# Performance work log

Measured on AMD Instinct MI355X. Metric: run time of the kernel, lower is better.

Reference implementation:

```python
import jax, jax.numpy as jnp
import numpy as np

B, T = 16, 100
MCL = 100      # MAX_CODE_LEN
D_IN = 200     # input_dim (= ques_encoding)
D_BERT = 768
KC = 50        # KC_one_hot_dim
KCD = 100      # kc_embed_dim
HID = 128
SCALE_BERT = 100
TW = 0.5       # QPALA_config.total_attention_weight
BTW = 0.5      # BLAA_config.total_attention_weight


def setup_inputs():
    key = jax.random.key(0)
    ks = jax.random.split(key, 20)
    f32 = jnp.float32
    # composite input feature vector: [ques_enc | code2vec idx | bert | time | score | kc one-hot]
    rnn_first = (jax.random.uniform(ks[0], (B, T, D_IN)) < 0.1).astype(f32)
    c2v = jax.random.randint(ks[1], (B, T, 3 * MCL), 0, 10000).astype(f32)
    bert = jax.random.normal(ks[2], (B, T, D_BERT), f32)
    time_f = jax.random.uniform(ks[3], (B, T, 10), f32)
    score_f = jax.random.uniform(ks[4], (B, T, 2), f32)
    kc = (jax.random.uniform(ks[5], (B, T, KC)) < 0.15).astype(f32)
    x = jnp.concatenate([rnn_first, c2v, bert, time_f, score_f, kc], axis=2)  # [B,T,1330]
    s = 0.05
    p = lambda k, shp: jax.random.normal(k, shp, f32) * s
    return dict(
        x=x,
        node_emb=p(ks[6], (10002, 100)),
        path_emb=p(ks[7], (20002, 100)),
        Wb=p(ks[8], (SCALE_BERT, D_BERT)), bb=jnp.zeros((SCALE_BERT,), f32),
        Wna=p(ks[9], (500, 500)), bna=jnp.zeros((500,), f32),
        Wia=p(ks[10], (KCD, 500)), bia=jnp.zeros((KCD,), f32),
        Wattn=p(ks[11], (1, 500)), battn=jnp.zeros((1,), f32),
        kc_emb=p(ks[12], (KC, KCD)),
        Wt=p(ks[13], (1, SCALE_BERT + KC + KCD)), bt=jnp.zeros((1,), f32),
        Wih=p(ks[14], (4 * HID, 950)), Whh=p(ks[15], (4 * HID, HID)),
        bih=jnp.zeros((4 * HID,), f32), bhh=jnp.zeros((4 * HID,), f32),
        Wfc=p(ks[16], (100, HID + KC + D_IN)), bfc=jnp.zeros((100,), f32),
    )


def _lstm(xseq, Wih, Whh, bih, bhh):
    # PyTorch LSTM, gate order i,f,g,o; batch_first
    bsz = xseq.shape[0]
    pre = jnp.einsum('btd,gd->btg', xseq, Wih) + bih + bhh  # [B,T,4H]

    def step(carry, g_in):
        h, c = carry
        g = g_in + h @ Whh.T
        i, f, gg, o = jnp.split(g, 4, axis=-1)
        c = jax.nn.sigmoid(f) * c + jax.nn.sigmoid(i) * jnp.tanh(gg)
        h = jax.nn.sigmoid(o) * jnp.tanh(c)
        return (h, c), h

    init = (jnp.zeros((bsz, HID), xseq.dtype), jnp.zeros((bsz, HID), xseq.dtype))
    _, hs = jax.lax.scan(step, init, jnp.swapaxes(pre, 0, 1))
    return jnp.swapaxes(hs, 0, 1)


def _forward(x, node_emb, path_emb, Wb, bb, Wna, bna, Wia, bia, Wattn, battn,
             kc_emb, Wt, bt, Wih, Whh, bih, bhh, Wfc, bfc):
    b, t = x.shape[0], x.shape[1]
    rnn_first = x[:, :, :D_IN]
    bert = x[:, :, 500:500 + D_BERT]
    kc_part = x[:, :, 1280:1280 + KC]
    c2v = x[:, :, D_IN:D_IN + 3 * MCL].reshape(b, t, MCL, 3).astype(jnp.int32)
    # gather embeddings + broadcast encoding -> full_embed [B,T,MCL,500]
    full = jnp.concatenate([
        node_emb[c2v[..., 0]], node_emb[c2v[..., 2]], path_emb[c2v[..., 1]],
        jnp.broadcast_to(rnn_first[:, :, None, :], (b, t, MCL, D_IN))], axis=3)
    bert_vec = bert @ Wb.T + bb  # [B,T,100]
    # non-interactive attention pooling (NB: original softmaxes over dim=1 = time)
    cw = jnp.tanh(full @ Wna.T + bna) @ Wattn.T + battn  # [B,T,MCL,1]
    aw = jax.nn.softmax(cw, axis=1)
    na = jnp.sum(full * aw, axis=2)  # [B,T,500]
    kcn = jnp.sum(kc_part, axis=2, keepdims=True)
    kcn = jnp.where(kcn == 0, 1.0, kcn)
    # interactive (KC) cross attention
    trans = full @ Wia.T + bia  # [B,T,MCL,KCD]
    Q = kc_part[..., None] * kc_emb[None, None]  # [B,T,KC,KCD]
    attn = jax.nn.softmax(jnp.einsum('btkd,btmd->btkm', Q, trans), axis=-1)
    Hm = jnp.einsum('btkm,btmd->btkd', attn, trans) * kc_part[..., None]
    ia = jnp.sum(Hm, axis=2) / kcn  # [B,T,KCD]
    rnn_input = jnp.concatenate([kc_part, rnn_first, ia, na, bert_vec], axis=2)  # [B,T,950]
    lstm_out = _lstm(rnn_input, Wih, Whh, bih, bhh)  # [B,T,HID]
    # per-time-step causal attention over lstm_out (vectorized form of the python loop)
    w = (jnp.concatenate([bert_vec, kc_part, ia], axis=2) @ Wt.T + bt)[..., 0]  # [B,T]
    mask = jnp.tril(jnp.ones((t, t), bool))
    logits = jnp.where(mask[None], w[:, None, :], -1e30)
    cattn = jax.nn.softmax(logits, axis=-1)  # [B,T,T]
    cur = jnp.einsum('bij,bjh->bih', cattn, lstm_out)
    attended = lstm_out * (1.0 - TW)
    attended = attended.at[:, 0].set(lstm_out[:, 0])
    idx = jnp.arange(t)
    addm = ((idx >= 1) & (idx <= t - 2)).astype(x.dtype)[None, :, None]
    attended = attended + cur * BTW * addm
    out = jax.nn.sigmoid(
        jnp.concatenate([rnn_first, kc_part, attended], axis=2) @ Wfc.T + bfc)
    return out  # [B,T,100]


def reference(x, node_emb, path_emb, Wb, bb, Wna, bna, Wia, bia, Wattn, battn,
              kc_emb, Wt, bt, Wih, Whh, bih, bhh, Wfc, bfc):
    return _forward(x, node_emb, path_emb, Wb, bb, Wna, bna, Wia, bia, Wattn, battn,
                    kc_emb, Wt, bt, Wih, Whh, bih, bhh, Wfc, bfc)
```

## Files before the change

### kernel.cpp

```cpp
#include <hip/hip_runtime.h>
#include <math.h>

typedef unsigned short ushort_t;
typedef unsigned char uchar_t;
typedef __attribute__((ext_vector_type(8))) short bf16x8;
typedef __attribute__((ext_vector_type(4))) float f32x4;

constexpr int CB = 16, CT = 100, CMCL = 100, CDIN = 200;
constexpr int CKC = 50, CHID = 128;
constexpr int XCH = 1330;
constexpr int NBT = CB * CT;
constexpr int NNODE = 10002, NPATH = 20002;
constexpr int TRS = 114;
constexpr int HSTR = 136;
constexpr int NT8_W = 1024;
constexpr int NTF_W = 384;
constexpr int PT8_W = 512;
constexpr int PTF_W = 256;
constexpr int XR_W  = 640;

__device__ __forceinline__ float frcp(float v){ return __builtin_amdgcn_rcpf(v); }
__device__ __forceinline__ float fsigmoid(float v){ return frcp(1.f + __expf(-v)); }
__device__ __forceinline__ float ftanh_(float v){
  float e = __expf(-2.f*fabsf(v));
  return copysignf((1.f - e) * frcp(1.f + e), v);
}
__device__ __forceinline__ float wredsum(float v){
  #pragma unroll
  for (int off = 32; off; off >>= 1) v += __shfl_xor(v, off);
  return v;
}
__device__ __forceinline__ float wredmax(float v){
  #pragma unroll
  for (int off = 32; off; off >>= 1) v = fmaxf(v, __shfl_xor(v, off));
  return v;
}
__device__ __forceinline__ ushort_t f2b(float f){
  union { float f; unsigned u; } c{f};
  return (ushort_t)((c.u + 0x7FFFu + ((c.u >> 16) & 1u)) >> 16);
}
__device__ __forceinline__ float b2f(unsigned hbits){
  union { unsigned u; float f; } c{hbits << 16};
  return c.f;
}
__device__ __forceinline__ void b8f(const ushort_t* p, float* o){
  uint4 v = *reinterpret_cast<const uint4*>(p);
  o[0]=b2f(v.x & 0xFFFFu); o[1]=b2f(v.x >> 16);
  o[2]=b2f(v.y & 0xFFFFu); o[3]=b2f(v.y >> 16);
  o[4]=b2f(v.z & 0xFFFFu); o[5]=b2f(v.z >> 16);
  o[6]=b2f(v.w & 0xFFFFu); o[7]=b2f(v.w >> 16);
}
__device__ __forceinline__ uchar_t ff8(float f){
  union { float f; unsigned u; } c{f};
  unsigned s = (c.u >> 24) & 0x80u;
  unsigned a = c.u & 0x7FFFFFFFu;
  a = a < 0x3C000000u ? 0x3C000000u : a;
  a = a + 0x0007FFFFu + ((a >> 20) & 1u);
  a = a > 0x43E00000u ? 0x43E00000u : a;
  return (uchar_t)(s | (((a >> 20) - 0x3C0u) & 0x7Fu));
}
__device__ __forceinline__ void f8x8f(uint2 p, float* o){
  #pragma unroll
  for (int h = 0; h < 2; ++h) {
    unsigned w = h ? p.y : p.x;
    unsigned d0 = (w & 0xFFu) | ((w & 0xFF00u) << 8);
    unsigned d1 = ((w >> 16) & 0xFFu) | ((w >> 8) & 0x00FF0000u);
    unsigned v0 = ((d0 & 0x00800080u) << 8) | (((d0 & 0x007F007Fu) << 4) + 0x3C003C00u);
    unsigned v1 = ((d1 & 0x00800080u) << 8) | (((d1 & 0x007F007Fu) << 4) + 0x3C003C00u);
    union { unsigned u; float f; } c0{v0 << 16}, c1{v0 & 0xFFFF0000u}, c2{v1 << 16}, c3{v1 & 0xFFFF0000u};
    o[4*h+0] = c0.f; o[4*h+1] = c1.f; o[4*h+2] = c2.f; o[4*h+3] = c3.f;
  }
}

struct GDesc {
  const float* A; const float* B; float* Cf; void* Cb;
  int lda, kOff, kMax, K, M, Npad, rbp, cb, nsplit, ldc, omode, blocks;
};
struct MegaArgs { GDesc d[6]; int nd; };

__global__ __launch_bounds__(256) void mega_gemm(MegaArgs args)
{
  constexpr int KS = 136;
  __shared__ ushort_t As[128*KS];
  __shared__ ushort_t Bs[128*KS];
  int id = blockIdx.x;
  int di = 0;
  while (di < args.nd-1 && id >= args.d[di].blocks) { id -= args.d[di].blocks; ++di; }
  GDesc g = args.d[di];
  const int per = g.rbp * g.cb;
  const int sp = id / per, r = id % per;
  const int xcd = r & 7, s2 = r >> 3;
  const int y = xcd + 8*(s2 / g.cb), cbi = s2 % g.cb;
  const int bm = y*128, bn = cbi*128;
  if (bm >= g.M) return;
  const int tid = threadIdx.x, lane = tid & 63, w = tid >> 6;
  const int wm = w & 1, wn = w >> 1;
  const int lr = lane & 15, lkq = lane >> 4;
  const int kbase = g.kOff + sp * g.K;
  const int hK = g.K >> 1;

  for (int f = tid; f < 128*hK; f += 256) {
    int row = f / hK, j2 = (f % hK)*2;
    int gm = bm + row;
    float2 va = make_float2(0.f,0.f);
    if (gm < g.M && kbase + j2 + 2 <= g.kMax)
      va = *reinterpret_cast<const float2*>(g.A + (long)gm*g.lda + kbase + j2);
    *reinterpret_cast<unsigned*>(&As[row*KS + j2]) = (unsigned)f2b(va.x) | ((unsigned)f2b(va.y)<<16);
    float2 vb = *reinterpret_cast<const float2*>(g.B + ((long)sp*g.Npad + bn + row)*g.K + j2);
    *reinterpret_cast<unsigned*>(&Bs[row*KS + j2]) = (unsigned)f2b(vb.x) | ((unsigned)f2b(vb.y)<<16);
  }
  const int padw = (128 - g.K) >> 1;
  for (int f = tid; f < 128*padw; f += 256) {
    int row = f / padw, jd = f % padw;
    *reinterpret_cast<unsigned*>(&As[row*KS + g.K + jd*2]) = 0u;
    *reinterpret_cast<unsigned*>(&Bs[row*KS + g.K + jd*2]) = 0u;
  }
  __syncthreads();

  f32x4 acc[4][4];
  #pragma unroll
  for (int i = 0; i < 4; ++i)
    #pragma unroll
    for (int j = 0; j < 4; ++j) acc[i][j] = f32x4{0.f,0.f,0.f,0.f};
  #pragma unroll
  for (int ks = 0; ks < 4; ++ks) {
    const int ko = ks*32 + lkq*8;
    bf16x8 af[4], bf[4];
    #pragma unroll
    for (int i = 0; i < 4; ++i)
      af[i] = *reinterpret_cast<const bf16x8*>(&As[(wm*64 + i*16 + lr)*KS + ko]);
    #pragma unroll
    for (int j = 0; j < 4; ++j)
      bf[j] = *reinterpret_cast<const bf16x8*>(&Bs[(wn*64 + j*16 + lr)*KS + ko]);
    #pragma unroll
    for (int i = 0; i < 4; ++i)
      #pragma unroll
      for (int j = 0; j < 4; ++j)
        acc[i][j] = __builtin_amdgcn_mfma_f32_16x16x32_bf16(af[i], bf[j], acc[i][j], 0, 0, 0);
  }
  #pragma unroll
  for (int i = 0; i < 4; ++i) {
    #pragma unroll
    for (int j = 0; j < 4; ++j) {
      #pragma unroll
      for (int rr = 0; rr < 4; ++rr) {
        int gr = bm + wm*64 + i*16 + lkq*4 + rr;
        int gc = bn + wn*64 + j*16 + lr;
        if (gr < g.M) {
          float v = acc[i][j][rr];
          if (g.omode == 2)      ((uchar_t*)g.Cb)[(long)gr * g.ldc + gc] = ff8(v);
          else if (g.omode == 1) ((ushort_t*)g.Cb)[(long)gr * g.ldc + gc] = f2b(v);
          else                   g.Cf[((long)sp*g.M + gr)*g.ldc + gc] = v;
        }
      }
    }
  }
}

constexpr long PK_E0 = 1024L*100;
constexpr long PK_E1 = PK_E0 + 384L*100;
constexpr long PK_E2 = PK_E1 + 512L*100;
constexpr long PK_E3 = PK_E2 + 256L*100;
constexpr long PK_E4 = PK_E3 + 2L*XR_W*100;
constexpr long PK_E5 = PK_E4 + 6L*128*128;
constexpr long PK_E6 = PK_E5 + 10L*512*96;
constexpr long PK_E7 = PK_E6 + 512;
constexpr long PK_E8 = PK_E7 + 378L*100;

__global__ void pack_all(
    const float* __restrict__ Wna, const float* __restrict__ Wia,
    const float* __restrict__ bna, const float* __restrict__ bia,
    const float* __restrict__ Wb, const float* __restrict__ Wih,
    const float* __restrict__ Wattn, const float* __restrict__ Wfc,
    float* __restrict__ Bn8, float* __restrict__ Bnb,
    float* __restrict__ Bp8, float* __restrict__ Bpb,
    float* __restrict__ XB2, float* __restrict__ bias_x,
    float* __restrict__ BertB, float* __restrict__ P2B,
    ushort_t* __restrict__ WAB, float* __restrict__ WfcT)
{
  long i = (long)blockIdx.x*256 + threadIdx.x;
  if (i < PK_E0) {
    int n = (int)(i / 100), k = (int)(i % 100);
    float v = 0.f;
    if (n < 500)                    v = Wna[(long)n*500 + k];
    else if (n >= 512 && n < 1012)  v = Wna[(long)(n-512)*500 + 100 + k];
    Bn8[i] = v;
  } else if (i < PK_E1) {
    long j = i - PK_E0;
    int n = (int)(j / 100), k = (int)(j % 100);
    float v = 0.f;
    if (n < 100)                    v = (k == n) ? 1.f : 0.f;
    else if (n >= 112 && n < 212)   v = Wia[(long)(n-112)*500 + k];
    else if (n >= 224 && n < 324)   v = Wia[(long)(n-224)*500 + 100 + k];
    Bnb[j] = v;
  } else if (i < PK_E2) {
    long j = i - PK_E1;
    int n = (int)(j / 100), k = (int)(j % 100);
    Bp8[j] = (n < 500) ? Wna[(long)n*500 + 200 + k] : 0.f;
  } else if (i < PK_E3) {
    long j = i - PK_E2;
    int n = (int)(j / 100), k = (int)(j % 100);
    float v = 0.f;
    if (n < 100)                    v = (k == n) ? 1.f : 0.f;
    else if (n >= 112 && n < 212)   v = Wia[(long)(n-112)*500 + 200 + k];
    Bpb[j] = v;
  } else if (i < PK_E4) {
    long j = i - PK_E3;
    if (j < XR_W) {
      float b = 0.f;
      if (j < 500) b = bna[j];
      else if (j >= 512 && j < 612) b = bia[j-512];
      bias_x[j] = b;
    }
    int s = (int)(j / (XR_W*100)), n = (int)((j / 100) % XR_W), k = (int)(j % 100);
    int k2 = s*100 + k;
    float v = 0.f;
    if (n < 500)                  v = Wna[(long)n*500 + 300 + k2];
    else if (n >= 512 && n < 612) v = Wia[(long)(n-512)*500 + 300 + k2];
    XB2[j] = v;
  } else if (i < PK_E5) {
    long j = i - PK_E4;
    int s = (int)(j / (128*128)), n = (int)((j / 128) % 128), k = (int)(j % 128);
    BertB[j] = (n < 100) ? Wb[(long)n*768 + s*128 + k] : 0.f;
  } else if (i < PK_E6) {
    long j = i - PK_E5;
    int s = (int)(j / (512*96)), n = (int)((j / 96) % 512), k = (int)(j % 96);
    int kg = s*96 + k;
    P2B[j] = (kg < 950) ? Wih[(long)n*950 + kg] : 0.f;
  } else if (i < PK_E7) {
    long j = i - PK_E6;
    WAB[j] = (j < 500) ? f2b(Wattn[j]) : (ushort_t)0;
  } else if (i < PK_E8) {
    long j = i - PK_E7;
    int o = (int)(j / 378), q = (int)(j % 378);
    WfcT[q*100 + o] = Wfc[j];
  }
}

__global__ __launch_bounds__(256) void reduce1(
    const float* __restrict__ xrP, const float* __restrict__ bias_x, ushort_t* __restrict__ XR,
    const float* __restrict__ bertP, const float* __restrict__ bb, float* __restrict__ rnn)
{
  int bt = blockIdx.x, tid = threadIdx.x;
  for (int c = tid; c < XR_W; c += 256) {
    float v = xrP[(long)bt*XR_W + c] + xrP[((long)NBT + bt)*XR_W + c] + bias_x[c];
    XR[(long)bt*XR_W + c] = f2b(v);
  }
  if (tid < 100) {
    float v = bb[tid];
    #pragma unroll
    for (int s = 0; s < 6; ++s) v += bertP[((long)s*NBT + bt)*128 + tid];
    rnn[(long)bt*950 + 850 + tid] = v;
  }
}

__global__ __launch_bounds__(512) void reduce_p2(
    const float* __restrict__ p2P, const float* __restrict__ bih, const float* __restrict__ bhh,
    ushort_t* __restrict__ P2)
{
  int bt = blockIdx.x, g = threadIdx.x;
  float v = bih[g] + bhh[g];
  #pragma unroll
  for (int s = 0; s < 10; ++s) v += p2P[((long)s*NBT + bt)*512 + g];
  int bq = bt / CT, tt = bt % CT;
  int q = g >> 7, rem = g & 127, ww = rem >> 4, lr2 = rem & 15;
  int lk2 = bq >> 2, rr = bq & 3;
  P2[((((long)tt*4 + q)*8 + ww)*4 + lk2)*64 + lr2*4 + rr] = f2b(v);
}

__global__ __launch_bounds__(256) void cw2_kernel(
    const float* __restrict__ x, const uchar_t* __restrict__ NT8,
    const uchar_t* __restrict__ PT8, const ushort_t* __restrict__ XR,
    const ushort_t* __restrict__ WAB,
    const float* __restrict__ battn, float* __restrict__ cwT)
{
  int bt = blockIdx.x, b = bt / CT, t = bt % CT;
  int tid = threadIdx.x, w = tid >> 6, lane = tid & 63;
  __shared__ int idx_s[300];
  for (int i = tid; i < 300; i += 256) idx_s[i] = (int)x[(long)bt*XCH + 200 + i];
  float rseg[8], wseg[8];
  b8f(XR + (long)bt*XR_W + lane*8, rseg);
  b8f(WAB + lane*8, wseg);
  __syncthreads();
  float bat = battn[0];

  uint2 A0, C0, P0, A1, C1, P1;
  auto issue = [&](int m, uint2& A, uint2& C, uint2& P){
    if (m < CMCL) {
      int ai = idx_s[3*m], pi = idx_s[3*m+1], ci = idx_s[3*m+2];
      A = *reinterpret_cast<const uint2*>(NT8 + (long)ai*NT8_W + lane*8);
      C = *reinterpret_cast<const uint2*>(NT8 + (long)ci*NT8_W + 512 + lane*8);
      P = *reinterpret_cast<const uint2*>(PT8 + (long)pi*PT8_W + lane*8);
    }
  };
  auto proc = [&](int m, const uint2& A, const uint2& C, const uint2& P){
    if (m >= CMCL) return;
    float fa[8], fc[8], fp[8];
    f8x8f(A, fa); f8x8f(C, fc); f8x8f(P, fp);
    float acc = 0.f;
    #pragma unroll
    for (int j = 0; j < 8; ++j)
      acc = fmaf(ftanh_(fa[j] + fc[j] + fp[j] + rseg[j]), wseg[j], acc);
    acc = wredsum(acc);
    if (lane == 0) cwT[((long)b*CMCL + m)*CT + t] = acc + bat;
  };

  issue(w, A0, C0, P0);
  for (int it = 0; it < 25; it += 2) {
    int m0 = w + it*4;
    issue(m0 + 4, A1, C1, P1);
    proc(m0, A0, C0, P0);
    issue(m0 + 8, A0, C0, P0);
    proc(m0 + 4, A1, C1, P1);
  }
}

__global__ void aw_kernel(const float* __restrict__ cwT, float* __restrict__ awT)
{
  int bm = blockIdx.x; int lane = threadIdx.x;
  const float* row = cwT + (long)bm * CT;
  bool h1 = lane < (CT - 64);
  float v0 = row[lane];
  float v1 = h1 ? row[64 + lane] : -3.0e38f;
  float mx = wredmax(fmaxf(v0, v1));
  float e0 = __expf(v0 - mx);
  float e1 = h1 ? __expf(v1 - mx) : 0.f;
  float s = wredsum(e0 + e1);
  float inv = frcp(s);
  awT[(long)bm*CT + lane] = e0 * inv;
  if (h1) awT[(long)bm*CT + 64 + lane] = e1 * inv;
}

__global__ __launch_bounds__(256) void fuse2_kernel(
    const float* __restrict__ x,
    const uchar_t* __restrict__ NTF, const uchar_t* __restrict__ PTF,
    const ushort_t* __restrict__ XR, const float* __restrict__ awT,
    const float* __restrict__ kc_emb, float* __restrict__ rnn,
    const float* __restrict__ Wt, const float* __restrict__ bt0, float* __restrict__ wbuf)
{
  int bt = blockIdx.x, b = bt / CT, t = bt % CT;
  int tid = threadIdx.x, w = tid >> 6, lane = tid & 63;
  int sub = lane >> 5, li = lane & 31;

  __shared__ ushort_t tr_s[100*TRS];
  __shared__ float nacc[4][344];
  __shared__ float ia_red[4][104];
  __shared__ float ia_f[100];
  __shared__ float aw_s[100];
  __shared__ int   idx_s[300];
  __shared__ float kcl[CKC];
  __shared__ int   act_k[CKC];
  __shared__ int   nact_s;
  __shared__ float kcn_s, awsum_s;

  for (int i = tid; i < 300; i += 256) idx_s[i] = (int)x[(long)bt*XCH + 200 + i];
  if (tid < 100) aw_s[tid] = awT[((long)b*CMCL + tid)*CT + t];
  if (tid < CKC) kcl[tid] = x[(long)bt*XCH + 1280 + tid];
  __syncthreads();
  if (tid == 0) {
    float kcn = 0.f; int na = 0;
    for (int k = 0; k < CKC; ++k) { float v = kcl[k]; kcn += v; if (v != 0.f) act_k[na++] = k; }
    nact_s = na; kcn_s = (kcn == 0.f) ? 1.f : kcn;
    float s = 0.f;
    for (int m = 0; m < CMCL; ++m) s += aw_s[m];
    awsum_s = s;
  }
  float rwseg[8];
  if (li >= 14 && li < 28) b8f(XR + (long)bt*XR_W + 512 + (li-14)*8, rwseg);
  __syncthreads();

  float na_a[8] = {}, na_c[8] = {}, na_p[8] = {};
  const bool gv = (li < 28);
  uint2 A0, C0, P0, A1, C1, P1;
  auto g_issue = [&](int m, uint2& A, uint2& C, uint2& P){
    if (m < CMCL && gv) {
      int ai = idx_s[3*m], pi = idx_s[3*m+1], ci = idx_s[3*m+2];
      int offA = li*8;
      int offC = li*8 + ((li < 14) ? 0 : 112);
      A = *reinterpret_cast<const uint2*>(NTF + (long)ai*NTF_W + offA);
      C = *reinterpret_cast<const uint2*>(NTF + (long)ci*NTF_W + offC);
      P = *reinterpret_cast<const uint2*>(PTF + (long)pi*PTF_W + offA);
    }
  };
  auto g_proc = [&](int m, const uint2& A, const uint2& C, const uint2& P){
    if (m >= CMCL || !gv) return;
    float fa[8], fc[8], fp[8];
    f8x8f(A, fa); f8x8f(C, fc); f8x8f(P, fp);
    if (li < 14) {
      float awm = aw_s[m];
      #pragma unroll
      for (int j = 0; j < 8; ++j) {
        na_a[j] = fmaf(awm, fa[j], na_a[j]);
        na_c[j] = fmaf(awm, fc[j], na_c[j]);
        na_p[j] = fmaf(awm, fp[j], na_p[j]);
      }
    } else {
      unsigned* d32 = reinterpret_cast<unsigned*>(&tr_s[m*TRS + (li-14)*8]);
      #pragma unroll
      for (int jj = 0; jj < 4; ++jj) {
        float lo = fa[2*jj]   + fc[2*jj]   + fp[2*jj]   + rwseg[2*jj];
        float hi = fa[2*jj+1] + fc[2*jj+1] + fp[2*jj+1] + rwseg[2*jj+1];
        d32[jj] = (unsigned)f2b(lo) | ((unsigned)f2b(hi) << 16);
      }
    }
  };
  const int mb = w*2 + sub;
  g_issue(mb, A0, C0, P0);
  for (int it = 0; it < 13; it += 2) {
    g_issue((it+1)*8 + mb, A1, C1, P1);
    g_proc(it*8 + mb, A0, C0, P0);
    g_issue((it+2)*8 + mb, A0, C0, P0);
    g_proc((it+1)*8 + mb, A1, C1, P1);
  }
  #pragma unroll
  for (int j = 0; j < 8; ++j) {
    na_a[j] += __shfl_xor(na_a[j], 32);
    na_c[j] += __shfl_xor(na_c[j], 32);
    na_p[j] += __shfl_xor(na_p[j], 32);
  }
  if (lane < 14) {
    #pragma unroll
    for (int j = 0; j < 8; ++j) {
      nacc[w][      lane*8 + j] = na_a[j];
      nacc[w][112 + lane*8 + j] = na_c[j];
      nacc[w][224 + lane*8 + j] = na_p[j];
    }
  }
  __syncthreads();

  for (int q = tid; q < 336; q += 256) {
    float v = nacc[0][q] + nacc[1][q] + nacc[2][q] + nacc[3][q];
    int seg = q / 112, col = q % 112;
    if (col < 100) rnn[(long)bt*950 + 350 + seg*100 + col] = v;
  }
  for (int q = tid; q < CDIN; q += 256) {
    float xv = x[(long)bt*XCH + q];
    rnn[(long)bt*950 + 50 + q] = xv;
    rnn[(long)bt*950 + 650 + q] = awsum_s * xv;
  }
  if (tid < CKC) rnn[(long)bt*950 + tid] = kcl[tid];

  float ia0 = 0.f, ia1 = 0.f;
  const bool vrow1 = lane < 36;
  const bool vpv   = lane < 50;
  const int nact = nact_s;
  const unsigned* tr32_0 = reinterpret_cast<const unsigned*>(&tr_s[lane*TRS]);
  const unsigned* tr32_1 = reinterpret_cast<const unsigned*>(&tr_s[(64+lane)*TRS]);
  const unsigned* tr32   = reinterpret_cast<const unsigned*>(tr_s);
  for (int ki = w; ki < nact; ki += 4) {
    int k = act_k[ki];
    float kck = kcl[k];
    const float* ke = kc_emb + (long)k*100;
    float s0 = 0.f, s1 = 0.f;
    #pragma unroll 5
    for (int dh = 0; dh < 50; ++dh) {
      float k0 = ke[2*dh], k1 = ke[2*dh+1];
      unsigned u0 = tr32_0[dh];
      s0 = fmaf(k0, b2f(u0 & 0xffffu), s0);
      s0 = fmaf(k1, b2f(u0 >> 16), s0);
      if (vrow1) {
        unsigned u1 = tr32_1[dh];
        s1 = fmaf(k0, b2f(u1 & 0xffffu), s1);
        s1 = fmaf(k1, b2f(u1 >> 16), s1);
      }
    }
    s0 *= kck; s1 *= kck;
    float mx = wredmax(fmaxf(s0, vrow1 ? s1 : -3.0e38f));
    float p0e = __expf(s0 - mx);
    float p1e = vrow1 ? __expf(s1 - mx) : 0.f;
    float sm = wredsum(p0e + p1e);
    float inv = kck * frcp(sm);
    p0e *= inv; p1e *= inv;
    #pragma unroll 4
    for (int m = 0; m < CMCL; ++m) {
      float pm = (m < 64) ? __shfl(p0e, m) : __shfl(p1e, m - 64);
      if (vpv) {
        unsigned u = tr32[m*57 + lane];
        ia0 = fmaf(pm, b2f(u & 0xffffu), ia0);
        ia1 = fmaf(pm, b2f(u >> 16), ia1);
      }
    }
  }
  if (vpv) { ia_red[w][2*lane] = ia0; ia_red[w][2*lane+1] = ia1; }
  __syncthreads();
  if (tid < 100) {
    float v = (ia_red[0][tid] + ia_red[1][tid] + ia_red[2][tid] + ia_red[3][tid]) * frcp(kcn_s);
    rnn[(long)bt*950 + 250 + tid] = v;
    ia_f[tid] = v;
  }
  __syncthreads();
  if (tid < 64) {
    float acc = 0.f;
    for (int i = tid; i < 250; i += 64) {
      float f;
      if (i < 100)      f = rnn[(long)bt*950 + 850 + i];
      else if (i < 150) f = kcl[i - 100];
      else              f = ia_f[i - 150];
      acc = fmaf(Wt[i], f, acc);
    }
    acc = wredsum(acc);
    if (tid == 0) wbuf[bt] = acc + bt0[0];
  }
}

__global__ __launch_bounds__(512) void lstm_mfma2(
    const ushort_t* __restrict__ P2,
    const float* __restrict__ Whh,
    float* __restrict__ lstm_out)
{
  const int tid = threadIdx.x, lane = tid & 63, w = tid >> 6;
  const int lr = lane & 15, lkq = lane >> 4;
  __shared__ ushort_t H[2][16 * HSTR];
  {
    ushort_t* hp = &H[0][0];
    for (int i = tid; i < 2*16*HSTR; i += 512) hp[i] = 0;
  }

  bf16x8 bw0[4], bw1[4], bw2[4], bw3[4];
  #pragma unroll
  for (int kk = 0; kk < 4; ++kk) {
    short s[8];
    const float* wp0 = Whh + (long)(0*128 + w*16 + lr) * 128 + kk*32 + lkq*8;
    const float* wp1 = Whh + (long)(1*128 + w*16 + lr) * 128 + kk*32 + lkq*8;
    const float* wp2 = Whh + (long)(2*128 + w*16 + lr) * 128 + kk*32 + lkq*8;
    const float* wp3 = Whh + (long)(3*128 + w*16 + lr) * 128 + kk*32 + lkq*8;
    #pragma unroll
    for (int j = 0; j < 8; ++j) s[j] = (short)f2b(wp0[j]);
    bw0[kk] = bf16x8{s[0],s[1],s[2],s[3],s[4],s[5],s[6],s[7]};
    #pragma unroll
    for (int j = 0; j < 8; ++j) s[j] = (short)f2b(wp1[j]);
    bw1[kk] = bf16x8{s[0],s[1],s[2],s[3],s[4],s[5],s[6],s[7]};
    #pragma unroll
    for (int j = 0; j < 8; ++j) s[j] = (short)f2b(wp2[j]);
    bw2[kk] = bf16x8{s[0],s[1],s[2],s[3],s[4],s[5],s[6],s[7]};
    #pragma unroll
    for (int j = 0; j < 8; ++j) s[j] = (short)f2b(wp3[j]);
    bw3[kk] = bf16x8{s[0],s[1],s[2],s[3],s[4],s[5],s[6],s[7]};
  }

  auto pptr = [&](int t, int q){
    return reinterpret_cast<const uint2*>(P2 + (((((long)t*4 + q)*8 + w)*4 + lkq)*64 + lr*4));
  };
  uint2 pc0 = *pptr(0,0), pc1 = *pptr(0,1), pc2 = *pptr(0,2), pc3 = *pptr(0,3);
  uint2 pn0, pn1, pn2, pn3;
  f32x4 c = {0.f,0.f,0.f,0.f};
  __syncthreads();

  int pb = 0;
  for (int t = 0; t < CT; ++t) {
    if (t + 1 < CT) { pn0 = *pptr(t+1,0); pn1 = *pptr(t+1,1); pn2 = *pptr(t+1,2); pn3 = *pptr(t+1,3); }
    bf16x8 a[4];
    #pragma unroll
    for (int kk = 0; kk < 4; ++kk)
      a[kk] = *reinterpret_cast<const bf16x8*>(&H[pb][lr*HSTR + kk*32 + lkq*8]);
    f32x4 acc0 = f32x4{ b2f(pc0.x & 0xffffu), b2f(pc0.x >> 16), b2f(pc0.y & 0xffffu), b2f(pc0.y >> 16) };
    f32x4 acc1 = f32x4{ b2f(pc1.x & 0xffffu), b2f(pc1.x >> 16), b2f(pc1.y & 0xffffu), b2f(pc1.y >> 16) };
    f32x4 acc2 = f32x4{ b2f(pc2.x & 0xffffu), b2f(pc2.x >> 16), b2f(pc2.y & 0xffffu), b2f(pc2.y >> 16) };
    f32x4 acc3 = f32x4{ b2f(pc3.x & 0xffffu), b2f(pc3.x >> 16), b2f(pc3.y & 0xffffu), b2f(pc3.y >> 16) };
    #pragma unroll
    for (int kk = 0; kk < 4; ++kk) {
      acc0 = __builtin_amdgcn_mfma_f32_16x16x32_bf16(a[kk], bw0[kk], acc0, 0,0,0);
      acc1 = __builtin_amdgcn_mfma_f32_16x16x32_bf16(a[kk], bw1[kk], acc1, 0,0,0);
      acc2 = __builtin_amdgcn_mfma_f32_16x16x32_bf16(a[kk], bw2[kk], acc2, 0,0,0);
      acc3 = __builtin_amdgcn_mfma_f32_16x16x32_bf16(a[kk], bw3[kk], acc3, 0,0,0);
    }
    #pragma unroll
    for (int r = 0; r < 4; ++r) {
      float ig = fsigmoid(acc0[r]);
      float fg = fsigmoid(acc1[r]);
      float gg = ftanh_(acc2[r]);
      float og = fsigmoid(acc3[r]);
      c[r] = fg*c[r] + ig*gg;
      float h = og * ftanh_(c[r]);
      int row = lkq*4 + r;
      H[pb^1][row*HSTR + w*16 + lr] = f2b(h);
      lstm_out[((long)row*CT + t)*128 + w*16 + lr] = h;
    }
    __syncthreads();
    pb ^= 1;
    pc0 = pn0; pc1 = pn1; pc2 = pn2; pc3 = pn3;
  }
}

__global__ __launch_bounds__(256) void final_kernel(
    const float* __restrict__ x, const float* __restrict__ wbuf,
    const float* __restrict__ lstm_out, const float* __restrict__ WfcT,
    const float* __restrict__ bfc, float* __restrict__ out)
{
  int bt = blockIdx.x; int b = bt / CT, i = bt % CT;
  int tid = threadIdx.x;
  __shared__ float p_s[CT];
  __shared__ float feat_s[384];
  if (tid < 64) {
    bool h1 = (64 + tid) < CT;
    float v0 = (tid <= i) ? wbuf[(long)b*CT + tid] : -3.0e38f;
    float v1 = (h1 && (64 + tid) <= i) ? wbuf[(long)b*CT + 64 + tid] : -3.0e38f;
    float mx = wredmax(fmaxf(v0, v1));
    float e0 = (tid <= i) ? __expf(v0 - mx) : 0.f;
    float e1 = (h1 && (64 + tid) <= i) ? __expf(v1 - mx) : 0.f;
    float s = wredsum(e0 + e1);
    float inv = frcp(s);
    p_s[tid] = e0 * inv;
    if (h1) p_s[64 + tid] = e1 * inv;
  }
  __syncthreads();
  if (tid < CHID) {
    float cur = 0.f;
    #pragma unroll 4
    for (int j = 0; j <= i; ++j) cur = fmaf(p_s[j], lstm_out[((long)b*CT + j)*CHID + tid], cur);
    float l = lstm_out[((long)b*CT + i)*CHID + tid];
    float att;
    if (i == 0) att = l;
    else { att = 0.5f * l; if (i <= CT - 2) att = fmaf(0.5f, cur, att); }
    feat_s[250 + tid] = att;
  }
  for (int q = tid; q < 250; q += 256)
    feat_s[q] = (q < 200) ? x[(long)bt*XCH + q] : x[(long)bt*XCH + 1280 + (q - 200)];
  __syncthreads();
  if (tid < 100) {
    float acc = bfc[tid];
    #pragma unroll 4
    for (int q = 0; q < 378; ++q) acc = fmaf(WfcT[q*100 + tid], feat_s[q], acc);
    out[(long)bt*100 + tid] = fsigmoid(acc);
  }
}

extern "C" void kernel_launch(void* const* d_in, const int* in_sizes, int n_in,
                              void* d_out, int out_size, void* d_ws, size_t ws_size,
                              hipStream_t stream) {
  (void)in_sizes; (void)n_in; (void)out_size; (void)ws_size;
  const float* x        = (const float*)d_in[0];
  const float* node_emb = (const float*)d_in[1];
  const float* path_emb = (const float*)d_in[2];
  const float* Wb       = (const float*)d_in[3];
  const float* bb       = (const float*)d_in[4];
  const float* Wna      = (const float*)d_in[5];
  const float* bna      = (const float*)d_in[6];
  const float* Wia      = (const float*)d_in[7];
  const float* bia      = (const float*)d_in[8];
  const float* Wattn    = (const float*)d_in[9];
  const float* battn    = (const float*)d_in[10];
  const float* kc_emb   = (const float*)d_in[11];
  const float* Wt       = (const float*)d_in[12];
  const float* bt0      = (const float*)d_in[13];
  const float* Wih      = (const float*)d_in[14];
  const float* Whh      = (const float*)d_in[15];
  const float* bih      = (const float*)d_in[16];
  const float* bhh      = (const float*)d_in[17];
  const float* Wfc      = (const float*)d_in[18];
  const float* bfc      = (const float*)d_in[19];
  float* out = (float*)d_out;

  char* cur = (char*)d_ws;
  auto alloc = [&](size_t bytes)->char* {
    char* p = cur; cur += (bytes + 255) & ~(size_t)255; return p;
  };
  uchar_t* NT8   = (uchar_t*)alloc((size_t)NNODE*NT8_W);
  uchar_t* NTF   = (uchar_t*)alloc((size_t)NNODE*NTF_W);
  uchar_t* PT8   = (uchar_t*)alloc((size_t)NPATH*PT8_W);
  uchar_t* PTF   = (uchar_t*)alloc((size_t)NPATH*PTF_W);
  ushort_t* XR   = (ushort_t*)alloc((size_t)NBT*XR_W*2);
  float* Bn8    = (float*)alloc((size_t)1024*100*4);
  float* Bnb    = (float*)alloc((size_t)384*100*4);
  float* Bp8    = (float*)alloc((size_t)512*100*4);
  float* Bpb    = (float*)alloc((size_t)256*100*4);
  float* XB2    = (float*)alloc((size_t)2*XR_W*100*4);
  float* BertB  = (float*)alloc((size_t)6*128*128*4);
  float* P2B    = (float*)alloc((size_t)10*512*96*4);
  float* bias_x = (float*)alloc((size_t)XR_W*4);
  ushort_t* WAB = (ushort_t*)alloc(512*2);
  float* cwT  = (float*)alloc((size_t)NBT*100*4);
  float* awT  = (float*)alloc((size_t)NBT*100*4);
  float* rnn  = (float*)alloc((size_t)NBT*950*4);
  char*  uni  = alloc((size_t)10*NBT*512*4);
  float* xrP   = (float*)uni;
  float* bertP = (float*)(uni + (size_t)2*NBT*XR_W*4);
  float* p2P   = (float*)uni;
  ushort_t* P2 = (ushort_t*)alloc((size_t)NBT*512*2);
  float* lstm = (float*)alloc((size_t)NBT*128*4);
  float* wbuf = (float*)alloc((size_t)NBT*4);
  float* WfcT = (float*)alloc((size_t)378*100*4);

  pack_all<<<(unsigned)((PK_E8 + 255)/256), 256, 0, stream>>>(
      Wna, Wia, bna, bia, Wb, Wih, Wattn, Wfc,
      Bn8, Bnb, Bp8, Bpb, XB2, bias_x, BertB, P2B, WAB, WfcT);

  {
    MegaArgs a{};
    a.nd = 6;
    a.d[0] = { node_emb, Bn8, nullptr, NT8,  100, 0, 100, 100, NNODE, 1024, 80, 8, 1, 1024, 2, 80*8 };
    a.d[1] = { node_emb, Bnb, nullptr, NTF,  100, 0, 100, 100, NNODE, 384,  80, 3, 1, 384,  2, 80*3 };
    a.d[2] = { path_emb, Bp8, nullptr, PT8,  100, 0, 100, 100, NPATH, 512, 160, 4, 1, 512,  2, 160*4 };
    a.d[3] = { path_emb, Bpb, nullptr, PTF,  100, 0, 100, 100, NPATH, 256, 160, 2, 1, 256,  2, 160*2 };
    a.d[4] = { x, BertB, bertP, nullptr, XCH, 500, 1268, 128, NBT, 128, 16, 1, 6, 128, 0, 16*1*6 };
    a.d[5] = { x, XB2,   xrP,   nullptr, XCH, 0,   200,  100, NBT, XR_W, 16, 5, 2, XR_W, 0, 16*5*2 };
    int total = 0;
    for (int i2 = 0; i2 < 6; ++i2) total += a.d[i2].blocks;
    mega_gemm<<<total, 256, 0, stream>>>(a);
  }
  reduce1<<<NBT, 256, 0, stream>>>(xrP, bias_x, XR, bertP, bb, rnn);

  cw2_kernel<<<NBT,256,0,stream>>>(x, NT8, PT8, XR, WAB, battn, cwT);
  aw_kernel<<<CB*CMCL,64,0,stream>>>(cwT, awT);
  fuse2_kernel<<<NBT,256,0,stream>>>(x, NTF, PTF, XR, awT, kc_emb, rnn, Wt, bt0, wbuf);

  {
    MegaArgs a{};
    a.nd = 1;
    a.d[0] = { rnn, P2B, p2P, nullptr, 950, 0, 950, 96, NBT, 512, 16, 4, 10, 512, 0, 16*4*10 };
    mega_gemm<<<a.d[0].blocks, 256, 0, stream>>>(a);
  }
  reduce_p2<<<NBT, 512, 0, stream>>>(p2P, bih, bhh, P2);

  lstm_mfma2<<<1,512,0,stream>>>(P2, Whh, lstm);
  final_kernel<<<NBT,256,0,stream>>>(x, wbuf, lstm, WfcT, bfc, out);
}
```

Before: 520.5 us.

## Merge score and fusion gathers into one kernel, stash gathered embeddings for weighting

The attention-score gather (cw2) and the fusion gather (fuse2) are merged into one kernel that issues both embedding-table gathers in the same software-pipelined loop. The raw gathered fp8 node/path rows are written to a new global scratch buffer E. A new naw kernel then reads E back and applies the softmax weights, which previously needed a second pass over the tables after the softmax. This is meant to overlap the two random-gather streams and drop the dependency that forced a separate gather after softmax. In exchange it adds a large intermediate write and read (about 54 MB) and enlarges the shared scratch allocation.

```diff
diff --git a/kernel.cpp b/kernel.cpp
--- a/kernel.cpp
+++ b/kernel.cpp
@@ -18,6 +18,7 @@
 constexpr int PT8_W = 512;
 constexpr int PTF_W = 256;
 constexpr int XR_W  = 640;
+constexpr int E_W   = 336;
 
 __device__ __forceinline__ float frcp(float v){ return __builtin_amdgcn_rcpf(v); }
 __device__ __forceinline__ float fsigmoid(float v){ return frcp(1.f + __expf(-v)); }
@@ -268,24 +269,49 @@
   P2[((((long)tt*4 + q)*8 + ww)*4 + lk2)*64 + lr2*4 + rr] = f2b(v);
 }
 
-__global__ __launch_bounds__(256) void cw2_kernel(
-    const float* __restrict__ x, const uchar_t* __restrict__ NT8,
-    const uchar_t* __restrict__ PT8, const ushort_t* __restrict__ XR,
-    const ushort_t* __restrict__ WAB,
-    const float* __restrict__ battn, float* __restrict__ cwT)
+__global__ __launch_bounds__(256) void cwfuse_kernel(
+    const float* __restrict__ x,
+    const uchar_t* __restrict__ NT8, const uchar_t* __restrict__ PT8,
+    const uchar_t* __restrict__ NTF, const uchar_t* __restrict__ PTF,
+    const ushort_t* __restrict__ XR, const ushort_t* __restrict__ WAB,
+    const float* __restrict__ battn, const float* __restrict__ kc_emb,
+    float* __restrict__ cwT, uchar_t* __restrict__ E, float* __restrict__ rnn)
 {
   int bt = blockIdx.x, b = bt / CT, t = bt % CT;
   int tid = threadIdx.x, w = tid >> 6, lane = tid & 63;
-  __shared__ int idx_s[300];
+  int sub = lane >> 5, li = lane & 31;
+
+  __shared__ ushort_t tr_s[100*TRS];
+  __shared__ float ia_red[4][104];
+  __shared__ int   idx_s[300];
+  __shared__ float kcl[CKC];
+  __shared__ int   act_k[CKC];
+  __shared__ int   nact_s;
+  __shared__ float kcn_s;
+
   for (int i = tid; i < 300; i += 256) idx_s[i] = (int)x[(long)bt*XCH + 200 + i];
-  float rseg[8], wseg[8];
+  if (tid < CKC) kcl[tid] = x[(long)bt*XCH + 1280 + tid];
+  __syncthreads();
+  if (tid == 0) {
+    float kcn = 0.f; int na = 0;
+    for (int k = 0; k < CKC; ++k) { float v = kcl[k]; kcn += v; if (v != 0.f) act_k[na++] = k; }
+    nact_s = na; kcn_s = (kcn == 0.f) ? 1.f : kcn;
+  }
+  float rseg[8], wseg[8], rwseg[8];
   b8f(XR + (long)bt*XR_W + lane*8, rseg);
   b8f(WAB + lane*8, wseg);
-  __syncthreads();
+  if (li >= 14 && li < 28) b8f(XR + (long)bt*XR_W + 512 + (li-14)*8, rwseg);
   float bat = battn[0];
 
-  uint2 A0, C0, P0, A1, C1, P1;
-  auto issue = [&](int m, uint2& A, uint2& C, uint2& P){
+  if (tid < CKC) rnn[(long)bt*950 + tid] = kcl[tid];
+  for (int q = tid; q < CDIN; q += 256) rnn[(long)bt*950 + 50 + q] = x[(long)bt*XCH + q];
+
+  const bool gv = (li < 28);
+  uint2 cA0,cC0,cP0, cA1,cC1,cP1;
+  uint2 fA0,fC0,fP0, fA1,fC1,fP1;
+
+  auto cw_issue = [&](int it, uint2& A, uint2& C, uint2& P){
+    int m = w + it*4;
     if (m < CMCL) {
       int ai = idx_s[3*m], pi = idx_s[3*m+1], ci = idx_s[3*m+2];
       A = *reinterpret_cast<const uint2*>(NT8 + (long)ai*NT8_W + lane*8);
@@ -293,86 +319,9 @@
       P = *reinterpret_cast<const uint2*>(PT8 + (long)pi*PT8_W + lane*8);
     }
   };
-  auto proc = [&](int m, const uint2& A, const uint2& C, const uint2& P){
-    if (m >= CMCL) return;
-    float fa[8], fc[8], fp[8];
-    f8x8f(A, fa); f8x8f(C, fc); f8x8f(P, fp);
-    float acc = 0.f;
-    #pragma unroll
-    for (int j = 0; j < 8; ++j)
-      acc = fmaf(ftanh_(fa[j] + fc[j] + fp[j] + rseg[j]), wseg[j], acc);
-    acc = wredsum(acc);
-    if (lane == 0) cwT[((long)b*CMCL + m)*CT + t] = acc + bat;
-  };
-
-  issue(w, A0, C0, P0);
-  for (int it = 0; it < 25; it += 2) {
-    int m0 = w + it*4;
-    issue(m0 + 4, A1, C1, P1);
-    proc(m0, A0, C0, P0);
-    issue(m0 + 8, A0, C0, P0);
-    proc(m0 + 4, A1, C1, P1);
-  }
-}
-
-__global__ void aw_kernel(const float* __restrict__ cwT, float* __restrict__ awT)
-{
-  int bm = blockIdx.x; int lane = threadIdx.x;
-  const float* row = cwT + (long)bm * CT;
-  bool h1 = lane < (CT - 64);
-  float v0 = row[lane];
-  float v1 = h1 ? row[64 + lane] : -3.0e38f;
-  float mx = wredmax(fmaxf(v0, v1));
-  float e0 = __expf(v0 - mx);
-  float e1 = h1 ? __expf(v1 - mx) : 0.f;
-  float s = wredsum(e0 + e1);
-  float inv = frcp(s);
-  awT[(long)bm*CT + lane] = e0 * inv;
-  if (h1) awT[(long)bm*CT + 64 + lane] = e1 * inv;
-}
-
-__global__ __launch_bounds__(256) void fuse2_kernel(
-    const float* __restrict__ x,
-    const uchar_t* __restrict__ NTF, const uchar_t* __restrict__ PTF,
-    const ushort_t* __restrict__ XR, const float* __restrict__ awT,
-    const float* __restrict__ kc_emb, float* __restrict__ rnn,
-    const float* __restrict__ Wt, const float* __restrict__ bt0, float* __restrict__ wbuf)
-{
-  int bt = blockIdx.x, b = bt / CT, t = bt % CT;
-  int tid = threadIdx.x, w = tid >> 6, lane = tid & 63;
-  int sub = lane >> 5, li = lane & 31;
-
-  __shared__ ushort_t tr_s[100*TRS];
-  __shared__ float nacc[4][344];
-  __shared__ float ia_red[4][104];
-  __shared__ float ia_f[100];
-  __shared__ float aw_s[100];
-  __shared__ int   idx_s[300];
-  __shared__ float kcl[CKC];
-  __shared__ int   act_k[CKC];
-  __shared__ int   nact_s;
-  __shared__ float kcn_s, awsum_s;
-
-  for (int i = tid; i < 300; i += 256) idx_s[i] = (int)x[(long)bt*XCH + 200 + i];
-  if (tid < 100) aw_s[tid] = awT[((long)b*CMCL + tid)*CT + t];
-  if (tid < CKC) kcl[tid] = x[(long)bt*XCH + 1280 + tid];
-  __syncthreads();
-  if (tid == 0) {
-    float kcn = 0.f; int na = 0;
-    for (int k = 0; k < CKC; ++k) { float v = kcl[k]; kcn += v; if (v != 0.f) act_k[na++] = k; }
-    nact_s = na; kcn_s = (kcn == 0.f) ? 1.f : kcn;
-    float s = 0.f;
-    for (int m = 0; m < CMCL; ++m) s += aw_s[m];
-    awsum_s = s;
-  }
-  float rwseg[8];
-  if (li >= 14 && li < 28) b8f(XR + (long)bt*XR_W + 512 + (li-14)*8, rwseg);
-  __syncthreads();
-
-  float na_a[8] = {}, na_c[8] = {}, na_p[8] = {};
-  const bool gv = (li < 28);
-  uint2 A0, C0, P0, A1, C1, P1;
-  auto g_issue = [&](int m, uint2& A, uint2& C, uint2& P){
+  auto fz_issue = [&](int it, uint2& A, uint2& C, uint2& P){
+    if (it >= 13) return;
+    int m = it*8 + w*2 + sub;
     if (m < CMCL && gv) {
       int ai = idx_s[3*m], pi = idx_s[3*m+1], ci = idx_s[3*m+2];
       int offA = li*8;
@@ -382,19 +331,30 @@
       P = *reinterpret_cast<const uint2*>(PTF + (long)pi*PTF_W + offA);
     }
   };
-  auto g_proc = [&](int m, const uint2& A, const uint2& C, const uint2& P){
-    if (m >= CMCL || !gv) return;
+  auto cw_proc = [&](int it, const uint2& A, const uint2& C, const uint2& P){
+    int m = w + it*4;
+    if (m >= CMCL) return;
     float fa[8], fc[8], fp[8];
     f8x8f(A, fa); f8x8f(C, fc); f8x8f(P, fp);
+    float acc = 0.f;
+    #pragma unroll
+    for (int j = 0; j < 8; ++j)
+      acc = fmaf(ftanh_(fa[j] + fc[j] + fp[j] + rseg[j]), wseg[j], acc);
+    acc = wredsum(acc);
+    if (lane == 0) cwT[((long)b*CMCL + m)*CT + t] = acc + bat;
+  };
+  auto fz_proc = [&](int it, const uint2& A, const uint2& C, const uint2& P){
+    if (it >= 13) return;
+    int m = it*8 + w*2 + sub;
+    if (m >= CMCL || !gv) return;
     if (li < 14) {
-      float awm = aw_s[m];
-      #pragma unroll
-      for (int j = 0; j < 8; ++j) {
-        na_a[j] = fmaf(awm, fa[j], na_a[j]);
-        na_c[j] = fmaf(awm, fc[j], na_c[j]);
-        na_p[j] = fmaf(awm, fp[j], na_p[j]);
-      }
+      uchar_t* e = E + ((long)bt*CMCL + m)*E_W;
+      *reinterpret_cast<uint2*>(e +        li*8) = A;
+      *reinterpret_cast<uint2*>(e + 112 +  li*8) = C;
+      *reinterpret_cast<uint2*>(e + 224 +  li*8) = P;
     } else {
+      float fa[8], fc[8], fp[8];
+      f8x8f(A, fa); f8x8f(C, fc); f8x8f(P, fp);
       unsigned* d32 = reinterpret_cast<unsigned*>(&tr_s[m*TRS + (li-14)*8]);
       #pragma unroll
       for (int jj = 0; jj < 4; ++jj) {
@@ -404,41 +364,15 @@
       }
     }
   };
-  const int mb = w*2 + sub;
-  g_issue(mb, A0, C0, P0);
-  for (int it = 0; it < 13; it += 2) {
-    g_issue((it+1)*8 + mb, A1, C1, P1);
-    g_proc(it*8 + mb, A0, C0, P0);
-    g_issue((it+2)*8 + mb, A0, C0, P0);
-    g_proc((it+1)*8 + mb, A1, C1, P1);
-  }
-  #pragma unroll
-  for (int j = 0; j < 8; ++j) {
-    na_a[j] += __shfl_xor(na_a[j], 32);
-    na_c[j] += __shfl_xor(na_c[j], 32);
-    na_p[j] += __shfl_xor(na_p[j], 32);
-  }
-  if (lane < 14) {
-    #pragma unroll
-    for (int j = 0; j < 8; ++j) {
-      nacc[w][      lane*8 + j] = na_a[j];
-      nacc[w][112 + lane*8 + j] = na_c[j];
-      nacc[w][224 + lane*8 + j] = na_p[j];
-    }
-  }
-  __syncthreads();
-
-  for (int q = tid; q < 336; q += 256) {
-    float v = nacc[0][q] + nacc[1][q] + nacc[2][q] + nacc[3][q];
-    int seg = q / 112, col = q % 112;
-    if (col < 100) rnn[(long)bt*950 + 350 + seg*100 + col] = v;
-  }
-  for (int q = tid; q < CDIN; q += 256) {
-    float xv = x[(long)bt*XCH + q];
-    rnn[(long)bt*950 + 50 + q] = xv;
-    rnn[(long)bt*950 + 650 + q] = awsum_s * xv;
-  }
-  if (tid < CKC) rnn[(long)bt*950 + tid] = kcl[tid];
+
+  cw_issue(0, cA0,cC0,cP0); fz_issue(0, fA0,fC0,fP0);
+  for (int it = 0; it < 25; it += 2) {
+    cw_issue(it+1, cA1,cC1,cP1); fz_issue(it+1, fA1,fC1,fP1);
+    cw_proc(it, cA0,cC0,cP0);    fz_proc(it, fA0,fC0,fP0);
+    cw_issue(it+2, cA0,cC0,cP0); fz_issue(it+2, fA0,fC0,fP0);
+    cw_proc(it+1, cA1,cC1,cP1);  fz_proc(it+1, fA1,fC1,fP1);
+  }
+  __syncthreads();
 
   float ia0 = 0.f, ia1 = 0.f;
   const bool vrow1 = lane < 36;
@@ -486,20 +420,77 @@
   if (tid < 100) {
     float v = (ia_red[0][tid] + ia_red[1][tid] + ia_red[2][tid] + ia_red[3][tid]) * frcp(kcn_s);
     rnn[(long)bt*950 + 250 + tid] = v;
-    ia_f[tid] = v;
-  }
+  }
+}
+
+__global__ void aw_kernel(const float* __restrict__ cwT, float* __restrict__ awT)
+{
+  int bm = blockIdx.x; int lane = threadIdx.x;
+  const float* row = cwT + (long)bm * CT;
+  bool h1 = lane < (CT - 64);
+  float v0 = row[lane];
+  float v1 = h1 ? row[64 + lane] : -3.0e38f;
+  float mx = wredmax(fmaxf(v0, v1));
+  float e0 = __expf(v0 - mx);
+  float e1 = h1 ? __expf(v1 - mx) : 0.f;
+  float s = wredsum(e0 + e1);
+  float inv = frcp(s);
+  awT[(long)bm*CT + lane] = e0 * inv;
+  if (h1) awT[(long)bm*CT + 64 + lane] = e1 * inv;
+}
+
+__global__ __launch_bounds__(256) void naw_kernel(
+    const float* __restrict__ x, const uchar_t* __restrict__ E,
+    const float* __restrict__ awT, float* __restrict__ rnn,
+    const float* __restrict__ Wt, const float* __restrict__ bt0, float* __restrict__ wbuf)
+{
+  int bt = blockIdx.x, b = bt / CT, t = bt % CT;
+  int tid = threadIdx.x, w = tid >> 6, lane = tid & 63;
+  __shared__ float aw_s[100];
+  __shared__ float nacc[4][344];
+  __shared__ float awsum_sh;
+  if (tid < 100) aw_s[tid] = awT[((long)b*CMCL + tid)*CT + t];
   __syncthreads();
   if (tid < 64) {
-    float acc = 0.f;
-    for (int i = tid; i < 250; i += 64) {
+    float s = (lane < 50) ? (aw_s[lane] + aw_s[50 + lane]) : 0.f;
+    s = wredsum(s);
+    if (lane == 0) awsum_sh = s;
+  }
+  const bool av = lane < 42;
+  float acc[8] = {};
+  for (int m = w; m < CMCL; m += 4) {
+    float awm = aw_s[m];
+    if (av) {
+      uint2 ev = *reinterpret_cast<const uint2*>(E + ((long)bt*CMCL + m)*E_W + lane*8);
+      float f[8]; f8x8f(ev, f);
+      #pragma unroll
+      for (int j = 0; j < 8; ++j) acc[j] = fmaf(awm, f[j], acc[j]);
+    }
+  }
+  if (av) {
+    #pragma unroll
+    for (int j = 0; j < 8; ++j) nacc[w][lane*8 + j] = acc[j];
+  }
+  __syncthreads();
+  for (int q = tid; q < 336; q += 256) {
+    float v = nacc[0][q] + nacc[1][q] + nacc[2][q] + nacc[3][q];
+    int seg = q / 112, col = q % 112;
+    if (col < 100) rnn[(long)bt*950 + 350 + seg*100 + col] = v;
+  }
+  float awsum = awsum_sh;
+  for (int q = tid; q < CDIN; q += 256)
+    rnn[(long)bt*950 + 650 + q] = awsum * x[(long)bt*XCH + q];
+  if (tid < 64) {
+    float acc2 = 0.f;
+    for (int i = lane; i < 250; i += 64) {
       float f;
       if (i < 100)      f = rnn[(long)bt*950 + 850 + i];
-      else if (i < 150) f = kcl[i - 100];
-      else              f = ia_f[i - 150];
-      acc = fmaf(Wt[i], f, acc);
-    }
-    acc = wredsum(acc);
-    if (tid == 0) wbuf[bt] = acc + bt0[0];
+      else if (i < 150) f = x[(long)bt*XCH + 1280 + (i - 100)];
+      else              f = rnn[(long)bt*950 + 250 + (i - 150)];
+      acc2 = fmaf(Wt[i], f, acc2);
+    }
+    acc2 = wredsum(acc2);
+    if (lane == 0) wbuf[bt] = acc2 + bt0[0];
   }
 }
 
@@ -672,9 +663,11 @@
   float* cwT  = (float*)alloc((size_t)NBT*100*4);
   float* awT  = (float*)alloc((size_t)NBT*100*4);
   float* rnn  = (float*)alloc((size_t)NBT*950*4);
-  char*  uni  = alloc((size_t)10*NBT*512*4);
+  size_t uniBytes = (size_t)NBT*CMCL*E_W;
+  char*  uni  = alloc(uniBytes);
   float* xrP   = (float*)uni;
   float* bertP = (float*)(uni + (size_t)2*NBT*XR_W*4);
+  uchar_t* E   = (uchar_t*)uni;
   float* p2P   = (float*)uni;
   ushort_t* P2 = (ushort_t*)alloc((size_t)NBT*512*2);
   float* lstm = (float*)alloc((size_t)NBT*128*4);
@@ -700,9 +693,9 @@
   }
   reduce1<<<NBT, 256, 0, stream>>>(xrP, bias_x, XR, bertP, bb, rnn);
 
-  cw2_kernel<<<NBT,256,0,stream>>>(x, NT8, PT8, XR, WAB, battn, cwT);
+  cwfuse_kernel<<<NBT,256,0,stream>>>(x, NT8, PT8, NTF, PTF, XR, WAB, battn, kc_emb, cwT, E, rnn);
   aw_kernel<<<CB*CMCL,64,0,stream>>>(cwT, awT);
-  fuse2_kernel<<<NBT,256,0,stream>>>(x, NTF, PTF, XR, awT, kc_emb, rnn, Wt, bt0, wbuf);
+  naw_kernel<<<NBT,256,0,stream>>>(x, E, awT, rnn, Wt, bt0, wbuf);
 
   {
     MegaArgs a{};
```

Measured after the change: 536.9 us. 3.2% more time.
